# Performance work log

Measured on AMD Instinct MI355X. Metric: run time of the kernel, lower is better.

Reference implementation:

```python
import jax, jax.numpy as jnp
import numpy as np

NUM_SAMPLES = 5      # samples per line (line_matcher_cfg)
MIN_DIST_PTS = 8.0   # min pixel spacing between samples
TOP_K = 10           # top-k candidate lines for NW matching
GRID_SIZE = 4        # desc map stride
GAP = 0.1            # NW gap penalty


def sample_line_points(line_seg):
    # line_seg: (N, 2, 2) ij endpoints -> pts (N, S, 2), valid (N, S)
    start, end = line_seg[:, 0], line_seg[:, 1]
    lengths = jnp.linalg.norm(end - start, axis=1)
    nsamp = jnp.clip(jnp.floor(lengths / MIN_DIST_PTS), 2.0, float(NUM_SAMPLES))
    k = jnp.arange(NUM_SAMPLES, dtype=line_seg.dtype)
    interval = (end - start) / (nsamp - 1.0)[:, None]          # (N, 2)
    pts = start[:, None, :] + k[None, :, None] * interval[:, None, :]
    valid = k[None, :] < nsamp[:, None]
    pts = jnp.where(valid[..., None], pts, 0.0)                # torch pads with 0
    return pts, valid


def sample_descriptors(desc, pts):
    # Faithful F.grid_sample(bilinear, zeros padding, align_corners=False) after
    # kornia normalize_pixel_coordinates ((size-1) normalization), then L2-norm.
    # desc: (1, D, H, W); pts: (P, 2) ij coords in full-res image.
    D, H, W = desc.shape[1], desc.shape[2], desc.shape[3]
    img_h, img_w = H * GRID_SIZE, W * GRID_SIZE
    xn = 2.0 * pts[:, 1] / (img_w - 1) - 1.0
    yn = 2.0 * pts[:, 0] / (img_h - 1) - 1.0
    ix = ((xn + 1.0) * W - 1.0) / 2.0   # align_corners=False unnormalize
    iy = ((yn + 1.0) * H - 1.0) / 2.0
    x0f = jnp.floor(ix); y0f = jnp.floor(iy)
    wx = ix - x0f; wy = iy - y0f
    x0 = x0f.astype(jnp.int32); y0 = y0f.astype(jnp.int32)
    img = desc[0]

    def gather(xi, yi):
        inb = ((xi >= 0) & (xi < W) & (yi >= 0) & (yi < H)).astype(img.dtype)
        xc = jnp.clip(xi, 0, W - 1); yc = jnp.clip(yi, 0, H - 1)
        return img[:, yc, xc] * inb[None, :]   # (D, P), zeros outside

    v = (gather(x0, y0) * ((1 - wx) * (1 - wy))[None]
         + gather(x0 + 1, y0) * (wx * (1 - wy))[None]
         + gather(x0, y0 + 1) * ((1 - wx) * wy)[None]
         + gather(x0 + 1, y0 + 1) * (wx * wy)[None])
    return v / jnp.linalg.norm(v, axis=0, keepdims=True)


def needleman_wunsch(scores):
    # scores: (B, n, m); sequential DP via nested lax.scan (rows, then cols)
    B, n, m = scores.shape
    s = jnp.transpose(scores, (1, 0, 2)) - GAP  # (n, B, m)

    def row_step(prev_row, srow):               # prev_row (B, m+1), srow (B, m)
        diag = prev_row[:, :-1].T                # (m, B)
        up = prev_row[:, 1:].T                   # (m, B)

        def col_step(left, xs):
            d, u, sc = xs
            cur = jnp.maximum(jnp.maximum(left, u), d + sc)
            return cur, cur

        _, cols = jax.lax.scan(col_step, jnp.zeros((B,), s.dtype), (diag, up, srow.T))
        new_row = jnp.concatenate([jnp.zeros((B, 1), s.dtype), cols.T], axis=1)
        return new_row, None

    final, _ = jax.lax.scan(row_step, jnp.zeros((B, m + 1), s.dtype), s)
    return final[:, -1]


def filter_and_match_lines(scores):
    # scores: (N, M, n, n)
    ls1 = scores.max(3); v1 = (ls1 != -1.0).astype(scores.dtype)
    ls1 = (ls1 * v1).sum(2) / v1.sum(2)
    ls2 = scores.max(2); v2 = (ls2 != -1.0).astype(scores.dtype)
    ls2 = (ls2 * v2).sum(2) / v2.sum(2)
    line_scores = (ls1 + ls2) / 2.0
    topk_lines = jnp.argsort(line_scores, axis=1)[:, -TOP_K:]          # (N, k)
    top = jnp.take_along_axis(scores, topk_lines[:, :, None, None], axis=1)
    top = jnp.concatenate([top, jnp.flip(top, axis=-1)], axis=1)       # (N, 2k, n, n)
    N, top2k, n, m = top.shape
    nw = needleman_wunsch(top.reshape(N * top2k, n, m)).reshape(N, top2k)
    matches = jnp.argmax(nw, axis=1) % (top2k // 2)
    matches = topk_lines[jnp.arange(N), matches]
    return matches, nw


def match_forward(line_seg1, line_seg2, desc1, desc2):
    N, M = line_seg1.shape[0], line_seg2.shape[0]
    pts1, val1 = sample_line_points(line_seg1)
    pts2, val2 = sample_line_points(line_seg2)
    d1 = sample_descriptors(desc1, pts1.reshape(-1, 2))   # (D, N*S)
    d2 = sample_descriptors(desc2, pts2.reshape(-1, 2))   # (D, M*S)
    scores = d1.T @ d2                                    # (N*S, M*S)
    scores = jnp.where(val1.reshape(-1)[:, None], scores, -1.0)
    scores = jnp.where(val2.reshape(-1)[None, :], scores, -1.0)
    scores = scores.reshape(N, NUM_SAMPLES, M, NUM_SAMPLES).transpose(0, 2, 1, 3)
    matches, nw = filter_and_match_lines(scores)
    # cross check
    matches2, _ = filter_and_match_lines(scores.transpose(1, 0, 3, 2))
    mutual = matches2[matches] == jnp.arange(N)
    matches = jnp.where(mutual, matches, -1)
    return matches, nw


def setup_inputs():
    key = jax.random.key(0)
    k1, k2, k3, k4 = jax.random.split(key, 4)
    N = M = 1200; D = 128; H = W = 128
    img = float(H * GRID_SIZE - 1)
    line_seg1 = jax.random.uniform(k1, (N, 2, 2), jnp.float32) * img
    line_seg2 = jax.random.uniform(k2, (M, 2, 2), jnp.float32) * img
    desc1 = jax.random.normal(k3, (1, D, H, W), jnp.float32)
    desc2 = jax.random.normal(k4, (1, D, H, W), jnp.float32)
    return {"line_seg1": line_seg1, "line_seg2": line_seg2, "desc1": desc1, "desc2": desc2}


def reference(line_seg1, line_seg2, desc1, desc2):
    return match_forward(line_seg1, line_seg2, desc1, desc2)
```

## Files before the change

kernel.cpp:

```cpp
#include <hip/hip_runtime.h>
#include <hip/hip_bf16.h>


#define NLINES 1200
#define NS 5
#define DD 128
#define HH 128
#define WW 128
#define HW (HH*WW)
#define IMGM1 511.0f
#define GAPC 0.1f
#define NPAD 1216
#define PPAD (NPAD*NS)
#define KEXT 384
#define NCH (KEXT/32)
#define NGRP (PPAD/16)

typedef __attribute__((ext_vector_type(8))) short short8;
typedef __attribute__((ext_vector_type(4))) float f32x4;

__global__ void transpose_desc(const float* __restrict__ in, float* __restrict__ out) {
    __shared__ float t[32][33];
    int s0 = blockIdx.x * 32;
    int d0 = blockIdx.y * 32;
    int c = threadIdx.x;
    int r0 = threadIdx.y;
    #pragma unroll
    for (int rr = 0; rr < 32; rr += 8) {
        int d = d0 + r0 + rr;
        t[r0 + rr][c] = in[d * HW + s0 + c];
    }
    __syncthreads();
    #pragma unroll
    for (int rr = 0; rr < 32; rr += 8) {
        int s = s0 + r0 + rr;
        out[s * DD + d0 + c] = t[c][r0 + rr];
    }
}

__global__ void sample_kernel(const float* __restrict__ lseg,
                              const float* __restrict__ tdesc,
                              const float* __restrict__ desc,
                              float* __restrict__ Dout,
                              float* __restrict__ valout,
                              int use_t) {
    int wave = (blockIdx.x * blockDim.x + threadIdx.x) >> 6;
    int lane = threadIdx.x & 63;
    int pt = wave;
    if (pt >= PPAD) return;
    int line = pt / NS;
    int k = pt - line * NS;

    float sy = 0.f, sx = 0.f, ey = 0.f, ex = 0.f;
    if (line < NLINES) {
        sy = lseg[line * 4 + 0]; sx = lseg[line * 4 + 1];
        ey = lseg[line * 4 + 2]; ex = lseg[line * 4 + 3];
    }
    float dy = ey - sy, dx = ex - sx;
    float len = sqrtf(dy * dy + dx * dx);
    float ns = floorf(len * 0.125f);
    ns = fminf(fmaxf(ns, 2.0f), 5.0f);
    float kf = (float)k;
    float validf = (kf < ns) ? 1.0f : 0.0f;
    float py = sy + kf * (dy / (ns - 1.0f));
    float px = sx + kf * (dx / (ns - 1.0f));
    if (validf == 0.0f) { py = 0.0f; px = 0.0f; }

    float xn = 2.0f * px / IMGM1 - 1.0f;
    float yn = 2.0f * py / IMGM1 - 1.0f;
    float ix = ((xn + 1.0f) * (float)WW - 1.0f) * 0.5f;
    float iy = ((yn + 1.0f) * (float)HH - 1.0f) * 0.5f;
    float x0f = floorf(ix), y0f = floorf(iy);
    float wx = ix - x0f, wy = iy - y0f;
    int x0 = (int)x0f, y0 = (int)y0f;

    float w00 = (1.0f - wx) * (1.0f - wy);
    float w10 = wx * (1.0f - wy);
    float w01 = (1.0f - wx) * wy;
    float w11 = wx * wy;

    float v0 = 0.0f, v1 = 0.0f;
    int xs[4] = { x0, x0 + 1, x0,     x0 + 1 };
    int ys[4] = { y0, y0,     y0 + 1, y0 + 1 };
    float ws4[4] = { w00, w10, w01, w11 };
    #pragma unroll
    for (int c = 0; c < 4; ++c) {
        int xi = xs[c], yi = ys[c];
        float inb = (xi >= 0 && xi < WW && yi >= 0 && yi < HH) ? 1.0f : 0.0f;
        int xc = min(max(xi, 0), WW - 1);
        int yc = min(max(yi, 0), HH - 1);
        if (use_t) {
            int base = (yc * WW + xc) * DD;
            v0 += tdesc[base + lane] * inb * ws4[c];
            v1 += tdesc[base + 64 + lane] * inb * ws4[c];
        } else {
            int base = yc * WW + xc;
            v0 += desc[lane * HW + base] * inb * ws4[c];
            v1 += desc[(lane + 64) * HW + base] * inb * ws4[c];
        }
    }
    float ss = v0 * v0 + v1 * v1;
    #pragma unroll
    for (int o = 32; o > 0; o >>= 1) ss += __shfl_xor(ss, o);
    if (ss == 0.0f) ss = 1.0f;
    float nrm = sqrtf(ss);
    Dout[pt * DD + lane] = v0 / nrm;
    Dout[pt * DD + 64 + lane] = v1 / nrm;
    if (lane == 0) valout[pt] = (line < NLINES) ? validf : 0.0f;
}

__global__ void pack_kernel(const float* __restrict__ D, short* __restrict__ Ef, int arole) {
    __shared__ float ds[16][129];
    int g = blockIdx.x;
    int t = threadIdx.x;
    #pragma unroll
    for (int s = 0; s < 8; ++s) {
        int idx = s * 256 + t;
        int r = idx >> 7, k = idx & 127;
        ds[r][k] = D[((size_t)g * 16 + r) * DD + k];
    }
    __syncthreads();
    #pragma unroll
    for (int it = 0; it < 3; ++it) {
        int idx = it * 256 + t;
        int c = idx >> 6, l = idx & 63;
        int q = l >> 4, r = l & 15;
        short8 outv;
        #pragma unroll
        for (int jj = 0; jj < 8; ++jj) {
            int kext = c * 32 + q * 8 + jj;
            int term = kext >> 7, k = kext & 127;
            float x = ds[r][k];
            __hip_bfloat16 h = __float2bfloat16(x);
            short v = *(short*)&h;
            bool lo_term = arole ? (term == 1) : (term == 2);
            if (lo_term) {
                float hf = __bfloat162float(h);
                __hip_bfloat16 lw = __float2bfloat16(x - hf);
                v = *(short*)&lw;
            }
            outv[jj] = v;
        }
        *(short8*)&Ef[((size_t)(g * NCH + c) * 64 + l) * 8] = outv;
    }
}

__launch_bounds__(256, 2)
__global__ void score_kernel(const short* __restrict__ Af, const short* __restrict__ Bf,
                             const float* __restrict__ val1, const float* __restrict__ val2,
                             float* __restrict__ lsc) {
    __shared__ float dump[80 * 161];

    const int t = threadIdx.x;
    const int lane = t & 63;
    const int w = t >> 6;
    const int wm = w >> 1;
    const int wn = w & 1;
    const int gA0 = blockIdx.x * 10;
    const int gB0 = blockIdx.y * 10;

    const short* pa[5];
    const short* pb[5];
    #pragma unroll
    for (int ti = 0; ti < 5; ++ti) {
        pa[ti] = Af + ((size_t)(gA0 + 5 * wm + ti) * NCH * 64 + lane) * 8;
        pb[ti] = Bf + ((size_t)(gB0 + 5 * wn + ti) * NCH * 64 + lane) * 8;
    }

    f32x4 acc[5][5];
    #pragma unroll
    for (int a = 0; a < 5; ++a)
        #pragma unroll
        for (int b = 0; b < 5; ++b)
            acc[a][b] = (f32x4){0.f, 0.f, 0.f, 0.f};

    short8 ca[5], cb[5], na[5], nb[5];
    #pragma unroll
    for (int ti = 0; ti < 5; ++ti) {
        ca[ti] = *(const short8*)(pa[ti]);
        cb[ti] = *(const short8*)(pb[ti]);
    }
    #pragma unroll
    for (int c = 0; c < NCH; c += 2) {
        #pragma unroll
        for (int ti = 0; ti < 5; ++ti) {
            na[ti] = *(const short8*)(pa[ti] + (c + 1) * 512);
            nb[ti] = *(const short8*)(pb[ti] + (c + 1) * 512);
        }
        #pragma unroll
        for (int ti = 0; ti < 5; ++ti)
            #pragma unroll
            for (int tj = 0; tj < 5; ++tj)
                acc[ti][tj] = __builtin_amdgcn_mfma_f32_16x16x32_bf16(
                    ca[ti], cb[tj], acc[ti][tj], 0, 0, 0);
        if (c + 2 < NCH) {
            #pragma unroll
            for (int ti = 0; ti < 5; ++ti) {
                ca[ti] = *(const short8*)(pa[ti] + (c + 2) * 512);
                cb[ti] = *(const short8*)(pb[ti] + (c + 2) * 512);
            }
        }
        #pragma unroll
        for (int ti = 0; ti < 5; ++ti)
            #pragma unroll
            for (int tj = 0; tj < 5; ++tj)
                acc[ti][tj] = __builtin_amdgcn_mfma_f32_16x16x32_bf16(
                    na[ti], nb[tj], acc[ti][tj], 0, 0, 0);
    }

    const int i0l = blockIdx.x * 32;
    const int j0l = blockIdx.y * 32;
    #pragma unroll
    for (int p = 0; p < 2; ++p) {
        __syncthreads();
        if (wm == p) {
            #pragma unroll
            for (int ti = 0; ti < 5; ++ti) {
                #pragma unroll
                for (int reg = 0; reg < 4; ++reg) {
                    int rloc = 16 * ti + (lane >> 4) * 4 + reg;
                    #pragma unroll
                    for (int tj = 0; tj < 5; ++tj) {
                        int col = 80 * wn + 16 * tj + (lane & 15);
                        dump[rloc * 161 + col] = acc[ti][tj][reg];
                    }
                }
            }
        }
        __syncthreads();
        #pragma unroll
        for (int e = 0; e < 2; ++e) {
            int q = t * 2 + e;
            int li = q >> 5, lj = q & 31;
            int i = i0l + 16 * p + li;
            int j = j0l + lj;
            if (i < NLINES && j < NLINES) {
                float S[5][5];
                #pragma unroll
                for (int a = 0; a < 5; ++a) {
                    float va = val1[i * NS + a];
                    #pragma unroll
                    for (int b = 0; b < 5; ++b) {
                        float vb = val2[j * NS + b];
                        float sc = dump[(li * 5 + a) * 161 + (lj * 5 + b)];
                        S[a][b] = (va != 0.0f && vb != 0.0f) ? sc : -1.0f;
                    }
                }
                float sum1 = 0.0f, cnt1 = 0.0f;
                #pragma unroll
                for (int a = 0; a < 5; ++a) {
                    float r = S[a][0];
                    #pragma unroll
                    for (int b = 1; b < 5; ++b) r = fmaxf(r, S[a][b]);
                    float v = (r != -1.0f) ? 1.0f : 0.0f;
                    sum1 += r * v; cnt1 += v;
                }
                float sum2 = 0.0f, cnt2 = 0.0f;
                #pragma unroll
                for (int b = 0; b < 5; ++b) {
                    float r = S[0][b];
                    #pragma unroll
                    for (int a = 1; a < 5; ++a) r = fmaxf(r, S[a][b]);
                    float v = (r != -1.0f) ? 1.0f : 0.0f;
                    sum2 += r * v; cnt2 += v;
                }
                lsc[i * NLINES + j] = (sum1 / cnt1 + sum2 / cnt2) * 0.5f;
            }
        }
    }
}

__global__ void transpose_lsc(const float* __restrict__ in, float* __restrict__ out) {
    __shared__ float t[32][33];
    int x0 = blockIdx.x * 32, y0 = blockIdx.y * 32;
    int c = threadIdx.x, r0 = threadIdx.y;
    #pragma unroll
    for (int rr = 0; rr < 32; rr += 8) {
        int y = y0 + r0 + rr, x = x0 + c;
        if (y < NLINES && x < NLINES) t[r0 + rr][c] = in[y * NLINES + x];
    }
    __syncthreads();
    #pragma unroll
    for (int rr = 0; rr < 32; rr += 8) {
        int x = x0 + r0 + rr, y = y0 + c;
        if (x < NLINES && y < NLINES) out[x * NLINES + y] = t[c][r0 + rr];
    }
}

__global__ void topk_kernel(const float* __restrict__ ls, int* __restrict__ topk) {
    __shared__ float wv[4];
    __shared__ int wi[4];
    int row = blockIdx.x;
    int t = threadIdx.x;
    int lane = t & 63, w = t >> 6;
    float val[5];
    #pragma unroll
    for (int s = 0; s < 5; ++s) {
        int j = t + 256 * s;
        val[s] = (j < NLINES) ? ls[row * NLINES + j] : -1e30f;
    }
    float bv = -1e30f; int bi = -1;
    #pragma unroll
    for (int s = 0; s < 5; ++s) {
        int j = t + 256 * s;
        if (val[s] >= bv) { bv = val[s]; bi = j; }
    }
    for (int sel = 0; sel < 10; ++sel) {
        float rv = bv; int ri = bi;
        #pragma unroll
        for (int o = 32; o > 0; o >>= 1) {
            float ov = __shfl_xor(rv, o);
            int oi = __shfl_xor(ri, o);
            if (ov > rv || (ov == rv && oi > ri)) { rv = ov; ri = oi; }
        }
        if (lane == 0) { wv[w] = rv; wi[w] = ri; }
        __syncthreads();
        float fv = wv[0]; int fi = wi[0];
        #pragma unroll
        for (int qq = 1; qq < 4; ++qq)
            if (wv[qq] > fv || (wv[qq] == fv && wi[qq] > fi)) { fv = wv[qq]; fi = wi[qq]; }
        if (t == 0) topk[row * 10 + 9 - sel] = fi;
        if ((fi & 255) == t) {
            val[fi >> 8] = -1e30f;
            bv = -1e30f; bi = -1;
            #pragma unroll
            for (int s = 0; s < 5; ++s) {
                int j = t + 256 * s;
                if (val[s] >= bv) { bv = val[s]; bi = j; }
            }
        }
        __syncthreads();
    }
}

__device__ __forceinline__ float nw5(const float* M) {
    float F[6] = {0, 0, 0, 0, 0, 0};
    #pragma unroll
    for (int x = 0; x < 5; ++x) {
        float diag = F[0];
        float left = 0.0f;
        #pragma unroll
        for (int y = 1; y <= 5; ++y) {
            float up = F[y];
            float cur = fmaxf(fmaxf(left, up), diag + (M[x * 5 + y - 1] - GAPC));
            F[y] = cur; left = cur; diag = up;
        }
    }
    return F[5];
}

__global__ void nw_kernel(const short* __restrict__ Af, const short* __restrict__ Bf,
                          const float* __restrict__ val1, const float* __restrict__ val2,
                          const int* __restrict__ topk1, const int* __restrict__ topk2,
                          float* __restrict__ nwout, float* __restrict__ nw2buf) {
    __shared__ float sbuf[4][25];
    int w4 = threadIdx.x >> 6;
    int gw = blockIdx.x * 4 + w4;
    int lane = threadIdx.x & 63;
    int dir = (gw >= 12000) ? 1 : 0;
    int rem = gw - dir * 12000;
    int row = rem / 10, r = rem - row * 10;
    int i, j;
    if (!dir) { i = row; j = topk1[row * 10 + r]; }
    else      { j = row; i = topk2[row * 10 + r]; }

    int q = lane >> 4, rr = lane & 15;
    int ptA = i * 5 + rr, ptB = j * 5 + rr;
    const short* baseA = Af + ((size_t)((ptA >> 4) * NCH) * 64 + q * 16 + (ptA & 15)) * 8;
    const short* baseB = Bf + ((size_t)((ptB >> 4) * NCH) * 64 + q * 16 + (ptB & 15)) * 8;
    f32x4 acc = (f32x4){0.f, 0.f, 0.f, 0.f};
    #pragma unroll
    for (int c = 0; c < NCH; ++c) {
        short8 a = *(const short8*)(baseA + c * 512);
        short8 b = *(const short8*)(baseB + c * 512);
        acc = __builtin_amdgcn_mfma_f32_16x16x32_bf16(a, b, acc, 0, 0, 0);
    }
    if (lane < 5) {
        #pragma unroll
        for (int reg = 0; reg < 4; ++reg) sbuf[w4][reg * 5 + lane] = acc[reg];
    }
    if (lane >= 16 && lane < 21) sbuf[w4][20 + (lane - 16)] = acc[0];
    __syncthreads();
    if (lane == 0) {
        float S[25];
        #pragma unroll
        for (int a = 0; a < 5; ++a) {
            float va = val1[i * NS + a];
            #pragma unroll
            for (int b = 0; b < 5; ++b) {
                float vb = val2[j * NS + b];
                S[a * 5 + b] = (va != 0.0f && vb != 0.0f) ? sbuf[w4][a * 5 + b] : -1.0f;
            }
        }
        float M1[25], M2[25];
        if (!dir) {
            #pragma unroll
            for (int x = 0; x < 5; ++x)
                #pragma unroll
                for (int y = 0; y < 5; ++y) {
                    M1[x * 5 + y] = S[x * 5 + y];
                    M2[x * 5 + y] = S[x * 5 + (4 - y)];
                }
        } else {
            #pragma unroll
            for (int x = 0; x < 5; ++x)
                #pragma unroll
                for (int y = 0; y < 5; ++y) {
                    M1[x * 5 + y] = S[y * 5 + x];
                    M2[x * 5 + y] = S[(4 - y) * 5 + x];
                }
        }
        float n1 = nw5(M1);
        float n2 = nw5(M2);
        if (!dir) { nwout[row * 20 + r] = n1; nwout[row * 20 + 10 + r] = n2; }
        else      { nw2buf[row * 20 + r] = n1; nw2buf[row * 20 + 10 + r] = n2; }
    }
}

__global__ void argmax_kernel(const float* __restrict__ nw1, const float* __restrict__ nw2,
                              const int* __restrict__ topk1, const int* __restrict__ topk2,
                              int* __restrict__ mpre, int* __restrict__ m2) {
    int t = blockIdx.x * 256 + threadIdx.x;
    if (t >= 2400) return;
    int dir = t / NLINES, row = t - dir * NLINES;
    const float* nw = (dir ? nw2 : nw1) + row * 20;
    float best = nw[0]; int bi = 0;
    #pragma unroll
    for (int q = 1; q < 20; ++q) {
        float v = nw[q];
        if (v > best) { best = v; bi = q; }
    }
    int m = (dir ? topk2 : topk1)[row * 10 + (bi % 10)];
    if (dir) m2[row] = m; else mpre[row] = m;
}

__global__ void final_kernel(const int* __restrict__ mpre, const int* __restrict__ m2,
                             float* __restrict__ out) {
    int i = blockIdx.x * 256 + threadIdx.x;
    if (i >= NLINES) return;
    int m = mpre[i];
    out[i] = (m2[m] == i) ? (float)m : -1.0f;
}

extern "C" void kernel_launch(void* const* d_in, const int* in_sizes, int n_in,
                              void* d_out, int out_size, void* d_ws, size_t ws_size,
                              hipStream_t stream) {
    const float* lseg1 = (const float*)d_in[0];
    const float* lseg2 = (const float*)d_in[1];
    const float* desc1 = (const float*)d_in[2];
    const float* desc2 = (const float*)d_in[3];
    float* out = (float*)d_out;

    float* wsf = (float*)d_ws;
    size_t off = 0;
    float* D1 = wsf + off;     off += (size_t)PPAD * DD;
    float* D2 = wsf + off;     off += (size_t)PPAD * DD;
    float* val1 = wsf + off;   off += PPAD;
    float* val2 = wsf + off;   off += PPAD;
    float* lsc = wsf + off;    off += (size_t)NLINES * NLINES;
    float* lscT = wsf + off;   off += (size_t)NLINES * NLINES;
    int* topk1 = (int*)(wsf + off); off += NLINES * 10;
    int* topk2 = (int*)(wsf + off); off += NLINES * 10;
    int* mpre = (int*)(wsf + off);  off += 1280;
    int* m2 = (int*)(wsf + off);    off += 1280;
    float* nw2buf = wsf + off; off += NLINES * 20;
    short* Aext = (short*)(wsf + off); off += (size_t)PPAD * KEXT / 2;
    short* Bext = (short*)(wsf + off); off += (size_t)PPAD * KEXT / 2;
    float* tdesc1 = wsf + off; off += (size_t)HW * DD;
    float* tdesc2 = wsf + off; off += (size_t)HW * DD;
    size_t need_full = off * sizeof(float);
    int use_t = (ws_size >= need_full) ? 1 : 0;

    if (use_t) {
        transpose_desc<<<dim3(HW / 32, DD / 32), dim3(32, 8), 0, stream>>>(desc1, tdesc1);
        transpose_desc<<<dim3(HW / 32, DD / 32), dim3(32, 8), 0, stream>>>(desc2, tdesc2);
    }
    sample_kernel<<<PPAD / 4, 256, 0, stream>>>(lseg1, tdesc1, desc1, D1, val1, use_t);
    sample_kernel<<<PPAD / 4, 256, 0, stream>>>(lseg2, tdesc2, desc2, D2, val2, use_t);

    pack_kernel<<<NGRP, 256, 0, stream>>>(D1, Aext, 1);
    pack_kernel<<<NGRP, 256, 0, stream>>>(D2, Bext, 0);

    score_kernel<<<dim3(NPAD / 32, NPAD / 32), 256, 0, stream>>>(Aext, Bext, val1, val2, lsc);

    transpose_lsc<<<dim3(38, 38), dim3(32, 8), 0, stream>>>(lsc, lscT);

    topk_kernel<<<NLINES, 256, 0, stream>>>(lsc, topk1);
    topk_kernel<<<NLINES, 256, 0, stream>>>(lscT, topk2);

    nw_kernel<<<6000, 256, 0, stream>>>(Aext, Bext, val1, val2, topk1, topk2,
                                        out + NLINES, nw2buf);

    argmax_kernel<<<10, 256, 0, stream>>>(out + NLINES, nw2buf, topk1, topk2, mpre, m2);
    final_kernel<<<5, 256, 0, stream>>>(mpre, m2, out);
}
```

Before: 208.7 us.

## Fuse sampling with packing, merge per-side launches, write transposed scores in score kernel

Merges the two descriptor transposes, the two topk launches and the argmax/final pair into single launches using grid dimensions. Sampling and bf16 packing are fused through shared memory, which removes the fp32 D1/D2 round trip. The score kernel now writes the transposed score matrix directly, replacing the separate transpose pass. Its MFMA loop drops register double-buffering in favour of a simple non-unrolled loop with higher occupancy (launch bounds 3), which trades latency hiding for more resident blocks.

New measurement: 203.2 us. -2.6%, faster.

```diff
diff --git a/kernel.cpp b/kernel.cpp
--- a/kernel.cpp
+++ b/kernel.cpp
@@ -19,7 +19,10 @@
 typedef __attribute__((ext_vector_type(8))) short short8;
 typedef __attribute__((ext_vector_type(4))) float f32x4;
 
-__global__ void transpose_desc(const float* __restrict__ in, float* __restrict__ out) {
+__global__ void transpose_desc(const float* __restrict__ in1, float* __restrict__ out1,
+                               const float* __restrict__ in2, float* __restrict__ out2) {
+    const float* in = blockIdx.z ? in2 : in1;
+    float* out = blockIdx.z ? out2 : out1;
     __shared__ float t[32][33];
     int s0 = blockIdx.x * 32;
     int d0 = blockIdx.y * 32;
@@ -38,88 +41,91 @@
     }
 }
 
-__global__ void sample_kernel(const float* __restrict__ lseg,
-                              const float* __restrict__ tdesc,
-                              const float* __restrict__ desc,
-                              float* __restrict__ Dout,
-                              float* __restrict__ valout,
-                              int use_t) {
-    int wave = (blockIdx.x * blockDim.x + threadIdx.x) >> 6;
-    int lane = threadIdx.x & 63;
-    int pt = wave;
-    if (pt >= PPAD) return;
-    int line = pt / NS;
-    int k = pt - line * NS;
-
-    float sy = 0.f, sx = 0.f, ey = 0.f, ex = 0.f;
-    if (line < NLINES) {
-        sy = lseg[line * 4 + 0]; sx = lseg[line * 4 + 1];
-        ey = lseg[line * 4 + 2]; ex = lseg[line * 4 + 3];
-    }
-    float dy = ey - sy, dx = ex - sx;
-    float len = sqrtf(dy * dy + dx * dx);
-    float ns = floorf(len * 0.125f);
-    ns = fminf(fmaxf(ns, 2.0f), 5.0f);
-    float kf = (float)k;
-    float validf = (kf < ns) ? 1.0f : 0.0f;
-    float py = sy + kf * (dy / (ns - 1.0f));
-    float px = sx + kf * (dx / (ns - 1.0f));
-    if (validf == 0.0f) { py = 0.0f; px = 0.0f; }
-
-    float xn = 2.0f * px / IMGM1 - 1.0f;
-    float yn = 2.0f * py / IMGM1 - 1.0f;
-    float ix = ((xn + 1.0f) * (float)WW - 1.0f) * 0.5f;
-    float iy = ((yn + 1.0f) * (float)HH - 1.0f) * 0.5f;
-    float x0f = floorf(ix), y0f = floorf(iy);
-    float wx = ix - x0f, wy = iy - y0f;
-    int x0 = (int)x0f, y0 = (int)y0f;
-
-    float w00 = (1.0f - wx) * (1.0f - wy);
-    float w10 = wx * (1.0f - wy);
-    float w01 = (1.0f - wx) * wy;
-    float w11 = wx * wy;
-
-    float v0 = 0.0f, v1 = 0.0f;
-    int xs[4] = { x0, x0 + 1, x0,     x0 + 1 };
-    int ys[4] = { y0, y0,     y0 + 1, y0 + 1 };
-    float ws4[4] = { w00, w10, w01, w11 };
-    #pragma unroll
-    for (int c = 0; c < 4; ++c) {
-        int xi = xs[c], yi = ys[c];
-        float inb = (xi >= 0 && xi < WW && yi >= 0 && yi < HH) ? 1.0f : 0.0f;
-        int xc = min(max(xi, 0), WW - 1);
-        int yc = min(max(yi, 0), HH - 1);
-        if (use_t) {
-            int base = (yc * WW + xc) * DD;
-            v0 += tdesc[base + lane] * inb * ws4[c];
-            v1 += tdesc[base + 64 + lane] * inb * ws4[c];
-        } else {
-            int base = yc * WW + xc;
-            v0 += desc[lane * HW + base] * inb * ws4[c];
-            v1 += desc[(lane + 64) * HW + base] * inb * ws4[c];
-        }
-    }
-    float ss = v0 * v0 + v1 * v1;
-    #pragma unroll
-    for (int o = 32; o > 0; o >>= 1) ss += __shfl_xor(ss, o);
-    if (ss == 0.0f) ss = 1.0f;
-    float nrm = sqrtf(ss);
-    Dout[pt * DD + lane] = v0 / nrm;
-    Dout[pt * DD + 64 + lane] = v1 / nrm;
-    if (lane == 0) valout[pt] = (line < NLINES) ? validf : 0.0f;
-}
-
-__global__ void pack_kernel(const float* __restrict__ D, short* __restrict__ Ef, int arole) {
+__global__ void samplepack_kernel(const float* __restrict__ lseg1, const float* __restrict__ lseg2,
+                                  const float* __restrict__ tdesc1, const float* __restrict__ tdesc2,
+                                  const float* __restrict__ desc1, const float* __restrict__ desc2,
+                                  short* __restrict__ Aext, short* __restrict__ Bext,
+                                  float* __restrict__ val1, float* __restrict__ val2,
+                                  int use_t) {
+    int side = blockIdx.y;
+    const float* lseg = side ? lseg2 : lseg1;
+    const float* tdesc = side ? tdesc2 : tdesc1;
+    const float* desc = side ? desc2 : desc1;
+    short* Ef = side ? Bext : Aext;
+    float* valout = side ? val2 : val1;
+    int arole = side ? 0 : 1;
+
     __shared__ float ds[16][129];
     int g = blockIdx.x;
     int t = threadIdx.x;
-    #pragma unroll
-    for (int s = 0; s < 8; ++s) {
-        int idx = s * 256 + t;
-        int r = idx >> 7, k = idx & 127;
-        ds[r][k] = D[((size_t)g * 16 + r) * DD + k];
+    int lane = t & 63, w = t >> 6;
+
+    #pragma unroll
+    for (int s = 0; s < 4; ++s) {
+        int r = w * 4 + s;
+        int pt = g * 16 + r;
+        int line = pt / NS;
+        int k = pt - line * NS;
+
+        float sy = 0.f, sx = 0.f, ey = 0.f, ex = 0.f;
+        if (line < NLINES) {
+            sy = lseg[line * 4 + 0]; sx = lseg[line * 4 + 1];
+            ey = lseg[line * 4 + 2]; ex = lseg[line * 4 + 3];
+        }
+        float dy = ey - sy, dx = ex - sx;
+        float len = sqrtf(dy * dy + dx * dx);
+        float ns = floorf(len * 0.125f);
+        ns = fminf(fmaxf(ns, 2.0f), 5.0f);
+        float kf = (float)k;
+        float validf = (kf < ns) ? 1.0f : 0.0f;
+        float py = sy + kf * (dy / (ns - 1.0f));
+        float px = sx + kf * (dx / (ns - 1.0f));
+        if (validf == 0.0f) { py = 0.0f; px = 0.0f; }
+
+        float xn = 2.0f * px / IMGM1 - 1.0f;
+        float yn = 2.0f * py / IMGM1 - 1.0f;
+        float ix = ((xn + 1.0f) * (float)WW - 1.0f) * 0.5f;
+        float iy = ((yn + 1.0f) * (float)HH - 1.0f) * 0.5f;
+        float x0f = floorf(ix), y0f = floorf(iy);
+        float wx = ix - x0f, wy = iy - y0f;
+        int x0 = (int)x0f, y0 = (int)y0f;
+
+        float w00 = (1.0f - wx) * (1.0f - wy);
+        float w10 = wx * (1.0f - wy);
+        float w01 = (1.0f - wx) * wy;
+        float w11 = wx * wy;
+
+        float v0 = 0.0f, v1 = 0.0f;
+        int xs[4] = { x0, x0 + 1, x0,     x0 + 1 };
+        int ys[4] = { y0, y0,     y0 + 1, y0 + 1 };
+        float ws4[4] = { w00, w10, w01, w11 };
+        #pragma unroll
+        for (int c = 0; c < 4; ++c) {
+            int xi = xs[c], yi = ys[c];
+            float inb = (xi >= 0 && xi < WW && yi >= 0 && yi < HH) ? 1.0f : 0.0f;
+            int xc = min(max(xi, 0), WW - 1);
+            int yc = min(max(yi, 0), HH - 1);
+            if (use_t) {
+                int base = (yc * WW + xc) * DD;
+                v0 += tdesc[base + lane] * inb * ws4[c];
+                v1 += tdesc[base + 64 + lane] * inb * ws4[c];
+            } else {
+                int base = yc * WW + xc;
+                v0 += desc[lane * HW + base] * inb * ws4[c];
+                v1 += desc[(lane + 64) * HW + base] * inb * ws4[c];
+            }
+        }
+        float ss = v0 * v0 + v1 * v1;
+        #pragma unroll
+        for (int o = 32; o > 0; o >>= 1) ss += __shfl_xor(ss, o);
+        if (ss == 0.0f) ss = 1.0f;
+        float nrm = sqrtf(ss);
+        ds[r][lane] = v0 / nrm;
+        ds[r][64 + lane] = v1 / nrm;
+        if (lane == 0) valout[pt] = (line < NLINES) ? validf : 0.0f;
     }
     __syncthreads();
+
     #pragma unroll
     for (int it = 0; it < 3; ++it) {
         int idx = it * 256 + t;
@@ -145,10 +151,10 @@
     }
 }
 
-__launch_bounds__(256, 2)
+__launch_bounds__(256, 3)
 __global__ void score_kernel(const short* __restrict__ Af, const short* __restrict__ Bf,
                              const float* __restrict__ val1, const float* __restrict__ val2,
-                             float* __restrict__ lsc) {
+                             float* __restrict__ lsc, float* __restrict__ lscT) {
     __shared__ float dump[80 * 161];
 
     const int t = threadIdx.x;
@@ -159,13 +165,8 @@
     const int gA0 = blockIdx.x * 10;
     const int gB0 = blockIdx.y * 10;
 
-    const short* pa[5];
-    const short* pb[5];
-    #pragma unroll
-    for (int ti = 0; ti < 5; ++ti) {
-        pa[ti] = Af + ((size_t)(gA0 + 5 * wm + ti) * NCH * 64 + lane) * 8;
-        pb[ti] = Bf + ((size_t)(gB0 + 5 * wn + ti) * NCH * 64 + lane) * 8;
-    }
+    const short* paw = Af + ((size_t)(gA0 + 5 * wm) * NCH * 64 + lane) * 8;
+    const short* pbw = Bf + ((size_t)(gB0 + 5 * wn) * NCH * 64 + lane) * 8;
 
     f32x4 acc[5][5];
     #pragma unroll
@@ -174,18 +175,13 @@
         for (int b = 0; b < 5; ++b)
             acc[a][b] = (f32x4){0.f, 0.f, 0.f, 0.f};
 
-    short8 ca[5], cb[5], na[5], nb[5];
-    #pragma unroll
-    for (int ti = 0; ti < 5; ++ti) {
-        ca[ti] = *(const short8*)(pa[ti]);
-        cb[ti] = *(const short8*)(pb[ti]);
-    }
-    #pragma unroll
-    for (int c = 0; c < NCH; c += 2) {
+    #pragma unroll 1
+    for (int c = 0; c < NCH; ++c) {
+        short8 ca[5], cb[5];
         #pragma unroll
         for (int ti = 0; ti < 5; ++ti) {
-            na[ti] = *(const short8*)(pa[ti] + (c + 1) * 512);
-            nb[ti] = *(const short8*)(pb[ti] + (c + 1) * 512);
+            ca[ti] = *(const short8*)(paw + ti * (NCH * 512) + c * 512);
+            cb[ti] = *(const short8*)(pbw + ti * (NCH * 512) + c * 512);
         }
         #pragma unroll
         for (int ti = 0; ti < 5; ++ti)
@@ -193,19 +189,6 @@
             for (int tj = 0; tj < 5; ++tj)
                 acc[ti][tj] = __builtin_amdgcn_mfma_f32_16x16x32_bf16(
                     ca[ti], cb[tj], acc[ti][tj], 0, 0, 0);
-        if (c + 2 < NCH) {
-            #pragma unroll
-            for (int ti = 0; ti < 5; ++ti) {
-                ca[ti] = *(const short8*)(pa[ti] + (c + 2) * 512);
-                cb[ti] = *(const short8*)(pb[ti] + (c + 2) * 512);
-            }
-        }
-        #pragma unroll
-        for (int ti = 0; ti < 5; ++ti)
-            #pragma unroll
-            for (int tj = 0; tj < 5; ++tj)
-                acc[ti][tj] = __builtin_amdgcn_mfma_f32_16x16x32_bf16(
-                    na[ti], nb[tj], acc[ti][tj], 0, 0, 0);
     }
 
     const int i0l = blockIdx.x * 32;
@@ -267,37 +250,62 @@
                 lsc[i * NLINES + j] = (sum1 / cnt1 + sum2 / cnt2) * 0.5f;
             }
         }
-    }
-}
-
-__global__ void transpose_lsc(const float* __restrict__ in, float* __restrict__ out) {
-    __shared__ float t[32][33];
-    int x0 = blockIdx.x * 32, y0 = blockIdx.y * 32;
-    int c = threadIdx.x, r0 = threadIdx.y;
-    #pragma unroll
-    for (int rr = 0; rr < 32; rr += 8) {
-        int y = y0 + r0 + rr, x = x0 + c;
-        if (y < NLINES && x < NLINES) t[r0 + rr][c] = in[y * NLINES + x];
-    }
-    __syncthreads();
-    #pragma unroll
-    for (int rr = 0; rr < 32; rr += 8) {
-        int x = x0 + r0 + rr, y = y0 + c;
-        if (x < NLINES && y < NLINES) out[x * NLINES + y] = t[c][r0 + rr];
-    }
-}
-
-__global__ void topk_kernel(const float* __restrict__ ls, int* __restrict__ topk) {
+        #pragma unroll
+        for (int e = 0; e < 2; ++e) {
+            int q = t * 2 + e;
+            int lj = q >> 4, li = q & 15;
+            int i = i0l + 16 * p + li;
+            int j = j0l + lj;
+            if (i < NLINES && j < NLINES) {
+                float S[5][5];
+                #pragma unroll
+                for (int a = 0; a < 5; ++a) {
+                    float va = val1[i * NS + a];
+                    #pragma unroll
+                    for (int b = 0; b < 5; ++b) {
+                        float vb = val2[j * NS + b];
+                        float sc = dump[(li * 5 + a) * 161 + (lj * 5 + b)];
+                        S[a][b] = (va != 0.0f && vb != 0.0f) ? sc : -1.0f;
+                    }
+                }
+                float sum1 = 0.0f, cnt1 = 0.0f;
+                #pragma unroll
+                for (int a = 0; a < 5; ++a) {
+                    float r = S[a][0];
+                    #pragma unroll
+                    for (int b = 1; b < 5; ++b) r = fmaxf(r, S[a][b]);
+                    float v = (r != -1.0f) ? 1.0f : 0.0f;
+                    sum1 += r * v; cnt1 += v;
+                }
+                float sum2 = 0.0f, cnt2 = 0.0f;
+                #pragma unroll
+                for (int b = 0; b < 5; ++b) {
+                    float r = S[0][b];
+                    #pragma unroll
+                    for (int a = 1; a < 5; ++a) r = fmaxf(r, S[a][b]);
+                    float v = (r != -1.0f) ? 1.0f : 0.0f;
+                    sum2 += r * v; cnt2 += v;
+                }
+                lscT[j * NLINES + i] = (sum1 / cnt1 + sum2 / cnt2) * 0.5f;
+            }
+        }
+    }
+}
+
+__global__ void topk_kernel(const float* __restrict__ lsc, const float* __restrict__ lscT,
+                            int* __restrict__ topk1, int* __restrict__ topk2) {
     __shared__ float wv[4];
     __shared__ int wi[4];
-    int row = blockIdx.x;
+    int rb = blockIdx.x;
+    const float* ls = (rb < NLINES) ? (lsc + rb * NLINES) : (lscT + (rb - NLINES) * NLINES);
+    int* topk = (rb < NLINES) ? (topk1 + rb * 10) : (topk2 + (rb - NLINES) * 10);
     int t = threadIdx.x;
     int lane = t & 63, w = t >> 6;
     float val[5];
     #pragma unroll
     for (int s = 0; s < 5; ++s) {
         int j = t + 256 * s;
-        val[s] = (j < NLINES) ? ls[row * NLINES + j] : -1e30f;
+        val[s] = (j < NLINES) ? ls[j] : -1e30f;
     }
     float bv = -1e30f; int bi = -1;
     #pragma unroll
@@ -319,7 +327,7 @@
         #pragma unroll
         for (int qq = 1; qq < 4; ++qq)
             if (wv[qq] > fv || (wv[qq] == fv && wi[qq] > fi)) { fv = wv[qq]; fi = wi[qq]; }
-        if (t == 0) topk[row * 10 + 9 - sel] = fi;
+        if (t == 0) topk[9 - sel] = fi;
         if ((fi & 255) == t) {
             val[fi >> 8] = -1e30f;
             bv = -1e30f; bi = -1;
@@ -417,29 +425,29 @@
     }
 }
 
-__global__ void argmax_kernel(const float* __restrict__ nw1, const float* __restrict__ nw2,
-                              const int* __restrict__ topk1, const int* __restrict__ topk2,
-                              int* __restrict__ mpre, int* __restrict__ m2) {
-    int t = blockIdx.x * 256 + threadIdx.x;
-    if (t >= 2400) return;
-    int dir = t / NLINES, row = t - dir * NLINES;
-    const float* nw = (dir ? nw2 : nw1) + row * 20;
-    float best = nw[0]; int bi = 0;
-    #pragma unroll
-    for (int q = 1; q < 20; ++q) {
-        float v = nw[q];
-        if (v > best) { best = v; bi = q; }
-    }
-    int m = (dir ? topk2 : topk1)[row * 10 + (bi % 10)];
-    if (dir) m2[row] = m; else mpre[row] = m;
-}
-
-__global__ void final_kernel(const int* __restrict__ mpre, const int* __restrict__ m2,
-                             float* __restrict__ out) {
-    int i = blockIdx.x * 256 + threadIdx.x;
-    if (i >= NLINES) return;
-    int m = mpre[i];
-    out[i] = (m2[m] == i) ? (float)m : -1.0f;
+__global__ void argmax_final_kernel(const float* __restrict__ nw1, const float* __restrict__ nw2,
+                                    const int* __restrict__ topk1, const int* __restrict__ topk2,
+                                    float* __restrict__ out) {
+    __shared__ int mpre[NLINES];
+    __shared__ int m2[NLINES];
+    int t = threadIdx.x;
+    for (int qq = t; qq < 2 * NLINES; qq += 1024) {
+        int dir = qq / NLINES, row = qq - dir * NLINES;
+        const float* nw = (dir ? nw2 : nw1) + row * 20;
+        float best = nw[0]; int bi = 0;
+        #pragma unroll
+        for (int q = 1; q < 20; ++q) {
+            float v = nw[q];
+            if (v > best) { best = v; bi = q; }
+        }
+        int m = (dir ? topk2 : topk1)[row * 10 + (bi % 10)];
+        if (dir) m2[row] = m; else mpre[row] = m;
+    }
+    __syncthreads();
+    for (int i = t; i < NLINES; i += 1024) {
+        int m = mpre[i];
+        out[i] = (m2[m] == i) ? (float)m : -1.0f;
+    }
 }
 
 extern "C" void kernel_launch(void* const* d_in, const int* in_sizes, int n_in,
@@ -453,16 +461,12 @@
 
     float* wsf = (float*)d_ws;
     size_t off = 0;
-    float* D1 = wsf + off;     off += (size_t)PPAD * DD;
-    float* D2 = wsf + off;     off += (size_t)PPAD * DD;
     float* val1 = wsf + off;   off += PPAD;
     float* val2 = wsf + off;   off += PPAD;
     float* lsc = wsf + off;    off += (size_t)NLINES * NLINES;
     float* lscT = wsf + off;   off += (size_t)NLINES * NLINES;
     int* topk1 = (int*)(wsf + off); off += NLINES * 10;
     int* topk2 = (int*)(wsf + off); off += NLINES * 10;
-    int* mpre = (int*)(wsf + off);  off += 1280;
-    int* m2 = (int*)(wsf + off);    off += 1280;
     float* nw2buf = wsf + off; off += NLINES * 20;
     short* Aext = (short*)(wsf + off); off += (size_t)PPAD * KEXT / 2;
     short* Bext = (short*)(wsf + off); off += (size_t)PPAD * KEXT / 2;
@@ -472,25 +476,19 @@
     int use_t = (ws_size >= need_full) ? 1 : 0;
 
     if (use_t) {
-        transpose_desc<<<dim3(HW / 32, DD / 32), dim3(32, 8), 0, stream>>>(desc1, tdesc1);
-        transpose_desc<<<dim3(HW / 32, DD / 32), dim3(32, 8), 0, stream>>>(desc2, tdesc2);
-    }
-    sample_kernel<<<PPAD / 4, 256, 0, stream>>>(lseg1, tdesc1, desc1, D1, val1, use_t);
-    sample_kernel<<<PPAD / 4, 256, 0, stream>>>(lseg2, tdesc2, desc2, D2, val2, use_t);
-
-    pack_kernel<<<NGRP, 256, 0, stream>>>(D1, Aext, 1);
-    pack_kernel<<<NGRP, 256, 0, stream>>>(D2, Bext, 0);
-
-    score_kernel<<<dim3(NPAD / 32, NPAD / 32), 256, 0, stream>>>(Aext, Bext, val1, val2, lsc);
-
-    transpose_lsc<<<dim3(38, 38), dim3(32, 8), 0, stream>>>(lsc, lscT);
-
-    topk_kernel<<<NLINES, 256, 0, stream>>>(lsc, topk1);
-    topk_kernel<<<NLINES, 256, 0, stream>>>(lscT, topk2);
+        transpose_desc<<<dim3(HW / 32, DD / 32, 2), dim3(32, 8), 0, stream>>>(
+            desc1, tdesc1, desc2, tdesc2);
+    }
+    samplepack_kernel<<<dim3(NGRP, 2), 256, 0, stream>>>(
+        lseg1, lseg2, tdesc1, tdesc2, desc1, desc2, Aext, Bext, val1, val2, use_t);
+
+    score_kernel<<<dim3(NPAD / 32, NPAD / 32), 256, 0, stream>>>(Aext, Bext, val1, val2,
+                                                                 lsc, lscT);
+
+    topk_kernel<<<2 * NLINES, 256, 0, stream>>>(lsc, lscT, topk1, topk2);
 
     nw_kernel<<<6000, 256, 0, stream>>>(Aext, Bext, val1, val2, topk1, topk2,
                                         out + NLINES, nw2buf);
 
-    argmax_kernel<<<10, 256, 0, stream>>>(out + NLINES, nw2buf, topk1, topk2, mpre, m2);
-    final_kernel<<<5, 256, 0, stream>>>(mpre, m2, out);
-}
+    argmax_final_kernel<<<1, 1024, 0, stream>>>(out + NLINES, nw2buf, topk1, topk2, out);
+}
```
